# Optimization experiments

Measured on AMD Instinct MI355X. Metric: run time of the kernel, lower is better.

The kernel has to match this reference:

```python
import jax, jax.numpy as jnp
import numpy as np

B, T, DIM = 8, 1024, 512
H, DK, L = 8, 64, 32          # heads, dim_key, rel_pos_length
DH = H * DK                    # dim_hidden = 512
DOUT = 512
EPS = 1e-5


def setup_inputs() -> dict:
    key = jax.random.key(0)
    ks = jax.random.split(key, 5)
    x = jax.random.normal(ks[0], (B, T, DIM), jnp.float32)
    Wqkv = jax.random.normal(ks[1], (3 * DH, DIM), jnp.float32) * (1.0 / np.sqrt(DIM))
    Wout = jax.random.normal(ks[2], (DOUT, DH), jnp.float32) * (1.0 / np.sqrt(DH))
    bout = jax.random.normal(ks[3], (DOUT,), jnp.float32) * 0.01
    rel_positions = jax.random.normal(ks[4], (2 * L - 1, DK), jnp.float32)
    bn_gamma = jnp.ones((DK,), jnp.float32)
    bn_beta = jnp.zeros((DK,), jnp.float32)
    return {"x": x, "Wqkv": Wqkv, "Wout": Wout, "bout": bout,
            "rel_positions": rel_positions, "bn_gamma": bn_gamma, "bn_beta": bn_beta}


def reference(x, Wqkv, Wout, bout, rel_positions, bn_gamma, bn_beta):
    b, t, f = x.shape
    # Conv1d(dim, 3*dim_hidden, 1, bias=False) on x.transpose(1,2) == pointwise matmul
    qkv = jnp.einsum('btf,of->bot', x, Wqkv)          # (b, 3*DH, t)
    q, k, v = jnp.split(qkv, 3, axis=1)
    q = q.reshape(b * H, DK, t)
    k = k.reshape(b * H, DK, t)
    v = v.reshape(b * H, DK, t)

    # linear-attention core: softmax over sequence for k, tiny DKxDK context
    k = jax.nn.softmax(k, axis=-1)
    context = jnp.einsum('ndt,net->nde', k, v)        # (n, DK, DK)
    content_out = jnp.einsum('nde,ndt->net', context, q)  # (n, DK, t); norm_queries=False

    # Relative-position path. Original builds one-hot It (t,t,2L-1) and
    # Pt = einsum('tir,rd->tid', It, rel_positions); then
    # St = einsum('ndt,tid->nit', q, Pt); rel = einsum('nit,net->net', St, v)
    #     = v * (sum_i St)[:,None,:].
    # sum_i Pt[t,i,d] = sum over valid band offsets of rel_positions -> band matmul.
    r = jnp.arange(-(L - 1), L)                       # (2L-1,)
    pos = jnp.arange(t)
    tgt = pos[:, None] + r[None, :]                   # i = x + r
    valid = ((tgt >= 0) & (tgt < t)).astype(x.dtype)  # (t, 2L-1)
    Psum = valid @ rel_positions                      # (t, DK) == Pt.sum(axis=1)
    S = jnp.einsum('ndt,td->nt', q, Psum)             # (n, t)
    rel = v * S[:, None, :]                           # (n, DK, t)

    # BatchNorm1d(DK), training-mode batch stats over (n, t), biased variance
    mu = jnp.mean(rel, axis=(0, 2), keepdims=True)
    var = jnp.mean((rel - mu) ** 2, axis=(0, 2), keepdims=True)
    rel = (rel - mu) * jax.lax.rsqrt(var + EPS) * bn_gamma[None, :, None] + bn_beta[None, :, None]

    out = (content_out + rel).reshape(b, DH, t)
    # Conv1d(dim_hidden, dim_out, 1) with bias
    return jnp.einsum('od,bdt->bot', Wout, out) + bout[None, :, None]
```

## Files before the change

kernel.cpp:

```cpp
#include <hip/hip_runtime.h>
#include <hip/hip_bf16.h>


typedef short bf16x8 __attribute__((ext_vector_type(8)));
typedef float f32x4 __attribute__((ext_vector_type(4)));

static __device__ __forceinline__ unsigned short f2bf(float f) {
  __hip_bfloat16 h = __float2bfloat16(f);
  return *reinterpret_cast<unsigned short*>(&h);
}
static __device__ __forceinline__ float bf2f(unsigned short u) {
  union { unsigned int i; float f; } c; c.i = ((unsigned int)u) << 16;
  return c.f;
}
static __device__ __forceinline__ void gl_lds16(const unsigned short* g, unsigned short* l) {
  __builtin_amdgcn_global_load_lds((const __attribute__((address_space(1))) unsigned int*)g,
                                   (__attribute__((address_space(3))) unsigned int*)l,
                                   16, 0, 0);
}

__global__ __launch_bounds__(256) void cast_all(const float* __restrict__ x,
                                                const float* __restrict__ wqkv,
                                                const float* __restrict__ wout,
                                                unsigned short* __restrict__ xb,
                                                unsigned short* __restrict__ wqkvb,
                                                unsigned short* __restrict__ woutb) {
  int j = blockIdx.x * 256 + threadIdx.x;
  const float* src; unsigned short* dst;
  if (j < 1048576) { src = x; dst = xb; }
  else if (j < 1245184) { j -= 1048576; src = wqkv; dst = wqkvb; }
  else { j -= 1245184; src = wout; dst = woutb; }
  float4 v = ((const float4*)src)[j];
  ushort4 o = {f2bf(v.x), f2bf(v.y), f2bf(v.z), f2bf(v.w)};
  ((ushort4*)dst)[j] = o;
}


__global__ __launch_bounds__(256) void gemm_qkv(const unsigned short* __restrict__ A,
                                                const unsigned short* __restrict__ B,
                                                unsigned short* __restrict__ C) {
  __shared__ alignas(16) unsigned short As[4096];
  __shared__ alignas(16) unsigned short Bs[4096];
  const int tid = threadIdx.x;
  const int wave = tid >> 6, lane = tid & 63;
  const int bm = blockIdx.y * 128, bn = blockIdx.x * 128;
  const int wm = (wave >> 1) * 64, wn = (wave & 1) * 64;
  const int fr = lane & 15, cq = lane >> 4;
  const int ch0 = tid, ch1 = 256 + tid;
  const int r0 = ch0 >> 2, c0 = (ch0 & 3) ^ ((r0 >> 1) & 3);
  const int r1 = ch1 >> 2, c1 = (ch1 & 3) ^ ((r1 >> 1) & 3);
  unsigned short* la0 = As + (wave * 64) * 8;
  unsigned short* la1 = As + (256 + wave * 64) * 8;
  unsigned short* lb0 = Bs + (wave * 64) * 8;
  unsigned short* lb1 = Bs + (256 + wave * 64) * 8;
  const unsigned short* Ar0 = A + (size_t)(bm + r0) * 512 + c0 * 8;
  const unsigned short* Ar1 = A + (size_t)(bm + r1) * 512 + c1 * 8;
  const unsigned short* Br0 = B + (size_t)(bn + r0) * 512 + c0 * 8;
  const unsigned short* Br1 = B + (size_t)(bn + r1) * 512 + c1 * 8;
  int offA[4], offB[4];
#pragma unroll
  for (int i = 0; i < 4; ++i) {
    int ra = wm + i * 16 + fr;
    offA[i] = (ra * 4 + (cq ^ ((ra >> 1) & 3))) * 8;
    int rb = wn + i * 16 + fr;
    offB[i] = (rb * 4 + (cq ^ ((rb >> 1) & 3))) * 8;
  }
  f32x4 acc[4][4];
#pragma unroll
  for (int i = 0; i < 4; ++i)
#pragma unroll
    for (int j = 0; j < 4; ++j) acc[i][j] = (f32x4){0.f, 0.f, 0.f, 0.f};
  for (int k0 = 0; k0 < 512; k0 += 32) {
    __syncthreads();
    gl_lds16(Ar0 + k0, la0);
    gl_lds16(Ar1 + k0, la1);
    gl_lds16(Br0 + k0, lb0);
    gl_lds16(Br1 + k0, lb1);
    __builtin_amdgcn_s_waitcnt(0);
    __syncthreads();
    bf16x8 af[4], bq[4];
#pragma unroll
    for (int mi = 0; mi < 4; ++mi) af[mi] = *(const bf16x8*)(As + offA[mi]);
#pragma unroll
    for (int nj = 0; nj < 4; ++nj) bq[nj] = *(const bf16x8*)(Bs + offB[nj]);
#pragma unroll
    for (int mi = 0; mi < 4; ++mi)
#pragma unroll
      for (int nj = 0; nj < 4; ++nj)
        acc[mi][nj] = __builtin_amdgcn_mfma_f32_16x16x32_bf16(af[mi], bq[nj], acc[mi][nj], 0, 0, 0);
  }
#pragma unroll
  for (int mi = 0; mi < 4; ++mi) {
    const int row0 = bm + wm + mi * 16 + (lane >> 4) * 4;
#pragma unroll
    for (int nj = 0; nj < 4; ++nj) {
      const int col = bn + wn + nj * 16 + fr;
#pragma unroll
      for (int rr = 0; rr < 4; ++rr)
        C[(size_t)(row0 + rr) * 8192 + col] = f2bf(acc[mi][nj][rr]);
    }
  }
}

__global__ __launch_bounds__(256) void gemm_out(const unsigned short* __restrict__ A,
                                                const unsigned short* __restrict__ B,
                                                const float* __restrict__ bias,
                                                float* __restrict__ out) {
  __shared__ alignas(16) unsigned short As[4096];
  __shared__ alignas(16) unsigned short Bs[4096];
  const int tid = threadIdx.x;
  const int wave = tid >> 6, lane = tid & 63;
  const int bm = blockIdx.y * 128, bn = blockIdx.x * 128;
  const int wm = (wave >> 1) * 64, wn = (wave & 1) * 64;
  const int fr = lane & 15, cq = lane >> 4;
  const int ch0 = tid, ch1 = 256 + tid;
  const int r0 = ch0 >> 2, c0 = (ch0 & 3) ^ ((r0 >> 1) & 3);
  const int r1 = ch1 >> 2, c1 = (ch1 & 3) ^ ((r1 >> 1) & 3);
  unsigned short* la0 = As + (wave * 64) * 8;
  unsigned short* la1 = As + (256 + wave * 64) * 8;
  unsigned short* lb0 = Bs + (wave * 64) * 8;
  unsigned short* lb1 = Bs + (256 + wave * 64) * 8;
  const unsigned short* Ar0 = A + (size_t)(bm + r0) * 512 + c0 * 8;
  const unsigned short* Ar1 = A + (size_t)(bm + r1) * 512 + c1 * 8;
  const unsigned short* Br0 = B + (size_t)(bn + r0) * 512 + c0 * 8;
  const unsigned short* Br1 = B + (size_t)(bn + r1) * 512 + c1 * 8;
  int offA[4], offB[4];
#pragma unroll
  for (int i = 0; i < 4; ++i) {
    int ra = wm + i * 16 + fr;
    offA[i] = (ra * 4 + (cq ^ ((ra >> 1) & 3))) * 8;
    int rb = wn + i * 16 + fr;
    offB[i] = (rb * 4 + (cq ^ ((rb >> 1) & 3))) * 8;
  }
  f32x4 acc[4][4];
#pragma unroll
  for (int i = 0; i < 4; ++i)
#pragma unroll
    for (int j = 0; j < 4; ++j) acc[i][j] = (f32x4){0.f, 0.f, 0.f, 0.f};
  for (int k0 = 0; k0 < 512; k0 += 32) {
    __syncthreads();
    gl_lds16(Ar0 + k0, la0);
    gl_lds16(Ar1 + k0, la1);
    gl_lds16(Br0 + k0, lb0);
    gl_lds16(Br1 + k0, lb1);
    __builtin_amdgcn_s_waitcnt(0);
    __syncthreads();
    bf16x8 af[4], bq[4];
#pragma unroll
    for (int mi = 0; mi < 4; ++mi) af[mi] = *(const bf16x8*)(As + offA[mi]);
#pragma unroll
    for (int nj = 0; nj < 4; ++nj) bq[nj] = *(const bf16x8*)(Bs + offB[nj]);
#pragma unroll
    for (int mi = 0; mi < 4; ++mi)
#pragma unroll
      for (int nj = 0; nj < 4; ++nj)
        acc[mi][nj] = __builtin_amdgcn_mfma_f32_16x16x32_bf16(af[mi], bq[nj], acc[mi][nj], 0, 0, 0);
  }
#pragma unroll
  for (int mi = 0; mi < 4; ++mi) {
    const int row0 = bm + wm + mi * 16 + (lane >> 4) * 4;
#pragma unroll
    for (int nj = 0; nj < 4; ++nj) {
      const int col = bn + wn + nj * 16 + fr;
      const int b = col >> 10, t = col & 1023;
#pragma unroll
      for (int rr = 0; rr < 4; ++rr)
        out[(size_t)b * 524288 + (size_t)(row0 + rr) * 1024 + t] = acc[mi][nj][rr] + bias[row0 + rr];
    }
  }
}

__global__ __launch_bounds__(256) void kstats(const unsigned short* __restrict__ qkv,
                                              float* __restrict__ lse) {
  const int tid = threadIdx.x;
  const int wave = tid >> 6, lane = tid & 63;
  const int r = blockIdx.x * 4 + wave;
  const int hd = r >> 3, b = r & 7;
  const unsigned short* row = qkv + (size_t)(512 + hd) * 8192 + b * 1024 + lane * 16;
  uint4 u0 = *(const uint4*)row;
  uint4 u1 = *(const uint4*)(row + 8);
  const unsigned short* us0 = (const unsigned short*)&u0;
  const unsigned short* us1 = (const unsigned short*)&u1;
  float f[16];
#pragma unroll
  for (int i = 0; i < 8; ++i) { f[i] = bf2f(us0[i]); f[8 + i] = bf2f(us1[i]); }
  float m = f[0];
#pragma unroll
  for (int i = 1; i < 16; ++i) m = fmaxf(m, f[i]);
#pragma unroll
  for (int off = 32; off; off >>= 1) m = fmaxf(m, __shfl_xor(m, off));
  float s = 0.f;
#pragma unroll
  for (int i = 0; i < 16; ++i) s += __expf(f[i] - m);
#pragma unroll
  for (int off = 32; off; off >>= 1) s += __shfl_xor(s, off);
  if (lane == 0) lse[r] = m + __logf(s);
}

__global__ __launch_bounds__(256) void psum_kernel(const float* __restrict__ relpos,
                                                   float* __restrict__ PsumT) {
  const int d = blockIdx.y;
  const int t = blockIdx.x * 256 + threadIdx.x;
  float acc = 0.f;
  for (int j = 0; j < 63; ++j) {
    int i = t + j - 31;
    float v = relpos[j * 64 + d];
    if (i >= 0 && i < 1024) acc += v;
  }
  PsumT[d * 1024 + t] = acc;
}

__global__ __launch_bounds__(256) void context_mfma(const unsigned short* __restrict__ qkv,
                                                    const float* __restrict__ lse,
                                                    float* __restrict__ ctx_part) {
  const int tc = blockIdx.x, n = blockIdx.y;
  const int b = n >> 3, h = n & 7;
  const int tid = threadIdx.x;
  const int wave = tid >> 6, lane = tid & 63;
  __shared__ float ls[64];
  __shared__ float ctx_l[64][68];
  if (tid < 64) ls[tid] = lse[(h * 64 + tid) * 8 + b];
  __syncthreads();
  const int fr = lane & 15, fk = (lane >> 4) * 8;
  const size_t colbase = (size_t)b * 1024 + tc * 256 + wave * 64;
  const unsigned short* kbase = qkv + (size_t)(512 + h * 64) * 8192 + colbase;
  const unsigned short* vbase = qkv + (size_t)(1024 + h * 64) * 8192 + colbase;
  f32x4 acc[4][4];
#pragma unroll
  for (int i = 0; i < 4; ++i)
#pragma unroll
    for (int j = 0; j < 4; ++j) acc[i][j] = (f32x4){0.f, 0.f, 0.f, 0.f};
#pragma unroll
  for (int ks = 0; ks < 2; ++ks) {
    const int tb = ks * 32 + fk;
    bf16x8 aF[4], bF[4];
#pragma unroll
    for (int dt = 0; dt < 4; ++dt) {
      const int row = dt * 16 + fr;
      bf16x8 kv = *(const bf16x8*)(kbase + (size_t)row * 8192 + tb);
      const float lv = ls[row];
      bf16x8 pv;
#pragma unroll
      for (int j = 0; j < 8; ++j)
        pv[j] = (short)f2bf(__expf(bf2f((unsigned short)kv[j]) - lv));
      aF[dt] = pv;
    }
#pragma unroll
    for (int et = 0; et < 4; ++et)
      bF[et] = *(const bf16x8*)(vbase + (size_t)(et * 16 + fr) * 8192 + tb);
#pragma unroll
    for (int dt = 0; dt < 4; ++dt)
#pragma unroll
      for (int et = 0; et < 4; ++et)
        acc[dt][et] = __builtin_amdgcn_mfma_f32_16x16x32_bf16(aF[dt], bF[et], acc[dt][et], 0, 0, 0);
  }
#pragma unroll
  for (int w = 0; w < 4; ++w) {
    if (wave == w) {
#pragma unroll
      for (int dt = 0; dt < 4; ++dt)
#pragma unroll
        for (int et = 0; et < 4; ++et) {
          const int col = et * 16 + fr;
#pragma unroll
          for (int rr = 0; rr < 4; ++rr) {
            const int rw = dt * 16 + (lane >> 4) * 4 + rr;
            if (w == 0) ctx_l[rw][col] = acc[dt][et][rr];
            else ctx_l[rw][col] += acc[dt][et][rr];
          }
        }
    }
    __syncthreads();
  }
  float* outp = ctx_part + ((size_t)tc * 64 + n) * 4096;
  for (int i = tid * 4; i < 4096; i += 1024) {
    const int rw = i >> 6, cc = i & 63;
    *(float4*)(outp + i) = *(const float4*)&ctx_l[rw][cc];
  }
}

__global__ __launch_bounds__(256) void reduce_ctx(const float* __restrict__ part,
                                                  float* __restrict__ ctx) {
  const int i4 = blockIdx.x * 256 + threadIdx.x;
  const float4* p = (const float4*)part;
  float4 a = p[i4], b = p[65536 + i4], c = p[131072 + i4], d = p[196608 + i4];
  float4 s = {a.x + b.x + c.x + d.x, a.y + b.y + c.y + d.y,
              a.z + b.z + c.z + d.z, a.w + b.w + c.w + d.w};
  ((float4*)ctx)[i4] = s;
}

__global__ __launch_bounds__(256) void s_stats(const unsigned short* __restrict__ qkv,
                                               const float* __restrict__ PsumT,
                                               float* __restrict__ S,
                                               float* __restrict__ part1,
                                               float* __restrict__ part2) {
  const int tc = blockIdx.x, n = blockIdx.y;
  const int b = n >> 3, h = n & 7;
  const int t0 = tc * 64;
  const int tid = threadIdx.x, wave = tid >> 6, lane = tid & 63;
  const int tg = lane & 7, rg = lane >> 3;
  __shared__ float swave[4][64];
  __shared__ float s_lds[64];
  const unsigned short* qbase = qkv + (size_t)(h * 64) * 8192 + b * 1024 + t0 + tg * 8;
  const float* pbase = PsumT + t0 + tg * 8;
  float acc[8] = {0.f};
#pragma unroll
  for (int i = 0; i < 2; ++i) {
    const int d = wave * 16 + i * 8 + rg;
    bf16x8 qv = *(const bf16x8*)(qbase + (size_t)d * 8192);
    float4 p0 = *(const float4*)(pbase + d * 1024);
    float4 p1 = *(const float4*)(pbase + d * 1024 + 4);
    float p[8] = {p0.x, p0.y, p0.z, p0.w, p1.x, p1.y, p1.z, p1.w};
#pragma unroll
    for (int j = 0; j < 8; ++j) acc[j] = fmaf(bf2f((unsigned short)qv[j]), p[j], acc[j]);
  }
#pragma unroll
  for (int off = 8; off < 64; off <<= 1)
#pragma unroll
    for (int j = 0; j < 8; ++j) acc[j] += __shfl_xor(acc[j], off);
  if (rg == 0) {
#pragma unroll
    for (int j = 0; j < 8; ++j) swave[wave][tg * 8 + j] = acc[j];
  }
  __syncthreads();
  if (tid < 64) {
    float s = swave[0][tid] + swave[1][tid] + swave[2][tid] + swave[3][tid];
    s_lds[tid] = s;
    S[(size_t)n * 1024 + t0 + tid] = s;
  }
  __syncthreads();
  const unsigned short* vbase = qkv + (size_t)(1024 + h * 64) * 8192 + b * 1024 + t0 + tg * 8;
  const int blk = n * 16 + tc;
  float sv[8];
#pragma unroll
  for (int j = 0; j < 8; ++j) sv[j] = s_lds[tg * 8 + j];
#pragma unroll
  for (int i = 0; i < 2; ++i) {
    const int e = wave * 16 + i * 8 + rg;
    bf16x8 vv = *(const bf16x8*)(vbase + (size_t)e * 8192);
    float a1 = 0.f, a2 = 0.f;
#pragma unroll
    for (int j = 0; j < 8; ++j) {
      float val = bf2f((unsigned short)vv[j]) * sv[j];
      a1 += val;
      a2 = fmaf(val, val, a2);
    }
#pragma unroll
    for (int off = 1; off < 8; off <<= 1) {
      a1 += __shfl_xor(a1, off);
      a2 += __shfl_xor(a2, off);
    }
    if (tg == 0) {
      part1[e * 1024 + blk] = a1;
      part2[e * 1024 + blk] = a2;
    }
  }
}

__global__ __launch_bounds__(256) void bn_reduce(const float* __restrict__ part1,
                                                 const float* __restrict__ part2,
                                                 const float* __restrict__ gamma,
                                                 const float* __restrict__ beta,
                                                 float* __restrict__ scale,
                                                 float* __restrict__ shift) {
  const int e = blockIdx.x;
  const int tid = threadIdx.x;
  float a1 = 0.f, a2 = 0.f;
#pragma unroll
  for (int i = 0; i < 4; ++i) {
    a1 += part1[e * 1024 + i * 256 + tid];
    a2 += part2[e * 1024 + i * 256 + tid];
  }
#pragma unroll
  for (int off = 32; off; off >>= 1) {
    a1 += __shfl_down(a1, off);
    a2 += __shfl_down(a2, off);
  }
  __shared__ float r1[4], r2[4];
  const int w = tid >> 6, lane = tid & 63;
  if (lane == 0) { r1[w] = a1; r2[w] = a2; }
  __syncthreads();
  if (tid == 0) {
    float s1 = r1[0] + r1[1] + r1[2] + r1[3];
    float s2 = r2[0] + r2[1] + r2[2] + r2[3];
    const float cnt = 65536.0f;
    float mu = s1 / cnt;
    float var = s2 / cnt - mu * mu;
    float sc = gamma[e] * rsqrtf(var + 1e-5f);
    scale[e] = sc;
    shift[e] = beta[e] - mu * sc;
  }
}

__global__ __launch_bounds__(256) void content_out_t(const unsigned short* __restrict__ qkv,
                                                     const float* __restrict__ ctx,
                                                     const float* __restrict__ S,
                                                     const float* __restrict__ scale,
                                                     const float* __restrict__ shift,
                                                     unsigned short* __restrict__ outT) {
  const int chunk = blockIdx.x, n = blockIdx.y;
  const int b = n >> 3, h = n & 7;
  const int t0 = chunk * 64;
  __shared__ float cs[4096];
  __shared__ alignas(16) unsigned short T[64][72];
  const float* cp = ctx + (size_t)n * 4096;
  for (int i = threadIdx.x * 4; i < 4096; i += 1024)
    *(float4*)&cs[i] = *(const float4*)&cp[i];
  __syncthreads();
  const int tid = threadIdx.x;
  const int e0 = (tid & 15) * 4;
  const int tq = (tid >> 4) * 4;
  const unsigned short* qbase = qkv + (size_t)(h * 64) * 8192 + b * 1024 + t0 + tq;
  float acc[4][4] = {{0.f}};
  for (int d = 0; d < 64; ++d) {
    float4 cv = *(const float4*)&cs[d * 64 + e0];
    ushort4 qu = *(const ushort4*)(qbase + (size_t)d * 8192);
    float qa[4] = {bf2f(qu.x), bf2f(qu.y), bf2f(qu.z), bf2f(qu.w)};
    float ca[4] = {cv.x, cv.y, cv.z, cv.w};
#pragma unroll
    for (int a = 0; a < 4; ++a)
#pragma unroll
      for (int c = 0; c < 4; ++c)
        acc[a][c] = fmaf(ca[a], qa[c], acc[a][c]);
  }
  float4 svv = *(const float4*)(S + (size_t)n * 1024 + t0 + tq);
  float sa[4] = {svv.x, svv.y, svv.z, svv.w};
  float4 scv = *(const float4*)(scale + e0);
  float4 shv = *(const float4*)(shift + e0);
  float sc[4] = {scv.x, scv.y, scv.z, scv.w};
  float sh[4] = {shv.x, shv.y, shv.z, shv.w};
#pragma unroll
  for (int a = 0; a < 4; ++a) {
    ushort4 vu = *(const ushort4*)(qkv + (size_t)(1024 + h * 64 + e0 + a) * 8192 + b * 1024 + t0 + tq);
    float va[4] = {bf2f(vu.x), bf2f(vu.y), bf2f(vu.z), bf2f(vu.w)};
#pragma unroll
    for (int c = 0; c < 4; ++c)
      T[tq + c][e0 + a] = f2bf(fmaf(va[c] * sa[c], sc[a], acc[a][c] + sh[a]));
  }
  __syncthreads();
  const int tl = tid >> 2, dq = (tid & 3) * 16;
  uint4 r0 = *(uint4*)&T[tl][dq];
  uint4 r1 = *(uint4*)&T[tl][dq + 8];
  unsigned short* op = outT + ((size_t)(b * 1024 + t0 + tl)) * 512 + h * 64 + dq;
  *(uint4*)op = r0;
  *(uint4*)(op + 8) = r1;
}

extern "C" void kernel_launch(void* const* d_in, const int* in_sizes, int n_in,
                              void* d_out, int out_size, void* d_ws, size_t ws_size,
                              hipStream_t stream) {
  const float* x       = (const float*)d_in[0];
  const float* Wqkv    = (const float*)d_in[1];
  const float* Wout    = (const float*)d_in[2];
  const float* bout    = (const float*)d_in[3];
  const float* relpos  = (const float*)d_in[4];
  const float* gamma   = (const float*)d_in[5];
  const float* beta    = (const float*)d_in[6];
  float* out = (float*)d_out;

  float* ws = (float*)d_ws;
  unsigned short* qkvb  = (unsigned short*)ws;
  float* p = ws + 6291456;
  unsigned short* xb    = (unsigned short*)p;  p += 2097152;
  unsigned short* wqkvb = (unsigned short*)p;  p += 393216;
  unsigned short* woutb = (unsigned short*)p;  p += 131072;
  float* ctx_part = p;  p += 1048576;
  float* ctx      = p;  p += 262144;
  float* PsumT    = p;  p += 65536;
  float* S        = p;  p += 65536;
  float* lse      = p;  p += 4096;
  float* part1    = p;  p += 65536;
  float* part2    = p;  p += 65536;
  float* scale    = p;  p += 64;
  float* shift    = p;  p += 64;
  unsigned short* outT = (unsigned short*)p;

  cast_all<<<5120, 256, 0, stream>>>(x, Wqkv, Wout, xb, wqkvb, woutb);
  psum_kernel<<<dim3(4, 64), 256, 0, stream>>>(relpos, PsumT);
  gemm_qkv<<<dim3(64, 12), 256, 0, stream>>>(wqkvb, xb, qkvb);
  kstats<<<1024, 256, 0, stream>>>(qkvb, lse);
  s_stats<<<dim3(16, 64), 256, 0, stream>>>(qkvb, PsumT, S, part1, part2);
  bn_reduce<<<64, 256, 0, stream>>>(part1, part2, gamma, beta, scale, shift);
  context_mfma<<<dim3(4, 64), 256, 0, stream>>>(qkvb, lse, ctx_part);
  reduce_ctx<<<256, 256, 0, stream>>>(ctx_part, ctx);
  content_out_t<<<dim3(16, 64), 256, 0, stream>>>(qkvb, ctx, S, scale, shift, outT);
  gemm_out<<<dim3(64, 4), 256, 0, stream>>>(woutb, outT, bout, out);
}
```

Baseline: 165.3 us.

## Merge independent launches into combined kernels and double GEMM K-tile to 64

```diff
diff --git a/kernel.cpp b/kernel.cpp
--- a/kernel.cpp
+++ b/kernel.cpp
@@ -19,75 +19,96 @@
                                    16, 0, 0);
 }
 
-__global__ __launch_bounds__(256) void cast_all(const float* __restrict__ x,
-                                                const float* __restrict__ wqkv,
-                                                const float* __restrict__ wout,
-                                                unsigned short* __restrict__ xb,
-                                                unsigned short* __restrict__ wqkvb,
-                                                unsigned short* __restrict__ woutb) {
-  int j = blockIdx.x * 256 + threadIdx.x;
-  const float* src; unsigned short* dst;
-  if (j < 1048576) { src = x; dst = xb; }
-  else if (j < 1245184) { j -= 1048576; src = wqkv; dst = wqkvb; }
-  else { j -= 1245184; src = wout; dst = woutb; }
-  float4 v = ((const float4*)src)[j];
-  ushort4 o = {f2bf(v.x), f2bf(v.y), f2bf(v.z), f2bf(v.w)};
-  ((ushort4*)dst)[j] = o;
+__global__ __launch_bounds__(256) void prep(const float* __restrict__ x,
+                                            const float* __restrict__ wqkv,
+                                            const float* __restrict__ wout,
+                                            const float* __restrict__ relpos,
+                                            unsigned short* __restrict__ xb,
+                                            unsigned short* __restrict__ wqkvb,
+                                            unsigned short* __restrict__ woutb,
+                                            float* __restrict__ PsumT) {
+  const int bx = blockIdx.x;
+  if (bx < 5120) {
+    int j = bx * 256 + threadIdx.x;
+    const float* src; unsigned short* dst;
+    if (j < 1048576) { src = x; dst = xb; }
+    else if (j < 1245184) { j -= 1048576; src = wqkv; dst = wqkvb; }
+    else { j -= 1245184; src = wout; dst = woutb; }
+    float4 v = ((const float4*)src)[j];
+    ushort4 o = {f2bf(v.x), f2bf(v.y), f2bf(v.z), f2bf(v.w)};
+    ((ushort4*)dst)[j] = o;
+  } else {
+    const int idx = bx - 5120;
+    const int d = idx >> 2;
+    const int t = (idx & 3) * 256 + threadIdx.x;
+    float acc = 0.f;
+    for (int j = 0; j < 63; ++j) {
+      int i = t + j - 31;
+      float v = relpos[j * 64 + d];
+      if (i >= 0 && i < 1024) acc += v;
+    }
+    PsumT[d * 1024 + t] = acc;
+  }
 }
 
 
 __global__ __launch_bounds__(256) void gemm_qkv(const unsigned short* __restrict__ A,
                                                 const unsigned short* __restrict__ B,
                                                 unsigned short* __restrict__ C) {
-  __shared__ alignas(16) unsigned short As[4096];
-  __shared__ alignas(16) unsigned short Bs[4096];
+  __shared__ alignas(16) unsigned short As[8192];
+  __shared__ alignas(16) unsigned short Bs[8192];
   const int tid = threadIdx.x;
   const int wave = tid >> 6, lane = tid & 63;
   const int bm = blockIdx.y * 128, bn = blockIdx.x * 128;
   const int wm = (wave >> 1) * 64, wn = (wave & 1) * 64;
   const int fr = lane & 15, cq = lane >> 4;
-  const int ch0 = tid, ch1 = 256 + tid;
-  const int r0 = ch0 >> 2, c0 = (ch0 & 3) ^ ((r0 >> 1) & 3);
-  const int r1 = ch1 >> 2, c1 = (ch1 & 3) ^ ((r1 >> 1) & 3);
-  unsigned short* la0 = As + (wave * 64) * 8;
-  unsigned short* la1 = As + (256 + wave * 64) * 8;
-  unsigned short* lb0 = Bs + (wave * 64) * 8;
-  unsigned short* lb1 = Bs + (256 + wave * 64) * 8;
-  const unsigned short* Ar0 = A + (size_t)(bm + r0) * 512 + c0 * 8;
-  const unsigned short* Ar1 = A + (size_t)(bm + r1) * 512 + c1 * 8;
-  const unsigned short* Br0 = B + (size_t)(bn + r0) * 512 + c0 * 8;
-  const unsigned short* Br1 = B + (size_t)(bn + r1) * 512 + c1 * 8;
-  int offA[4], offB[4];
-#pragma unroll
-  for (int i = 0; i < 4; ++i) {
-    int ra = wm + i * 16 + fr;
-    offA[i] = (ra * 4 + (cq ^ ((ra >> 1) & 3))) * 8;
-    int rb = wn + i * 16 + fr;
-    offB[i] = (rb * 4 + (cq ^ ((rb >> 1) & 3))) * 8;
-  }
+  const unsigned short* srcA[4];
+  const unsigned short* srcB[4];
+#pragma unroll
+  for (int j = 0; j < 4; ++j) {
+    const int s = tid + j * 256;
+    const int row = s >> 3, cp = s & 7;
+    const int c = cp ^ (row & 7);
+    srcA[j] = A + (size_t)(bm + row) * 512 + c * 8;
+    srcB[j] = B + (size_t)(bn + row) * 512 + c * 8;
+  }
+  int offA[4][2], offB[4][2];
+#pragma unroll
+  for (int i = 0; i < 4; ++i)
+#pragma unroll
+    for (int ks = 0; ks < 2; ++ks) {
+      int ra = wm + i * 16 + fr;
+      offA[i][ks] = (ra * 8 + ((ks * 4 + cq) ^ (ra & 7))) * 8;
+      int rb = wn + i * 16 + fr;
+      offB[i][ks] = (rb * 8 + ((ks * 4 + cq) ^ (rb & 7))) * 8;
+    }
   f32x4 acc[4][4];
 #pragma unroll
   for (int i = 0; i < 4; ++i)
 #pragma unroll
     for (int j = 0; j < 4; ++j) acc[i][j] = (f32x4){0.f, 0.f, 0.f, 0.f};
-  for (int k0 = 0; k0 < 512; k0 += 32) {
-    __syncthreads();
-    gl_lds16(Ar0 + k0, la0);
-    gl_lds16(Ar1 + k0, la1);
-    gl_lds16(Br0 + k0, lb0);
-    gl_lds16(Br1 + k0, lb1);
+  for (int k0 = 0; k0 < 512; k0 += 64) {
+    __syncthreads();
+#pragma unroll
+    for (int j = 0; j < 4; ++j) {
+      gl_lds16(srcA[j] + k0, As + (wave * 64 + j * 256) * 8);
+      gl_lds16(srcB[j] + k0, Bs + (wave * 64 + j * 256) * 8);
+    }
     __builtin_amdgcn_s_waitcnt(0);
     __syncthreads();
-    bf16x8 af[4], bq[4];
-#pragma unroll
-    for (int mi = 0; mi < 4; ++mi) af[mi] = *(const bf16x8*)(As + offA[mi]);
-#pragma unroll
-    for (int nj = 0; nj < 4; ++nj) bq[nj] = *(const bf16x8*)(Bs + offB[nj]);
-#pragma unroll
-    for (int mi = 0; mi < 4; ++mi)
-#pragma unroll
-      for (int nj = 0; nj < 4; ++nj)
-        acc[mi][nj] = __builtin_amdgcn_mfma_f32_16x16x32_bf16(af[mi], bq[nj], acc[mi][nj], 0, 0, 0);
+#pragma unroll
+    for (int ks = 0; ks < 2; ++ks) {
+      bf16x8 af[4], bq[4];
+#pragma unroll
+      for (int mi = 0; mi < 4; ++mi) af[mi] = *(const bf16x8*)(As + offA[mi][ks]);
+#pragma unroll
+      for (int nj = 0; nj < 4; ++nj) bq[nj] = *(const bf16x8*)(Bs + offB[nj][ks]);
+#pragma unroll
+      for (int mi = 0; mi < 4; ++mi)
+#pragma unroll
+        for (int nj = 0; nj < 4; ++nj)
+          acc[mi][nj] = __builtin_amdgcn_mfma_f32_16x16x32_bf16(af[mi], bq[nj], acc[mi][nj], 0, 0, 0);
+    }
   }
 #pragma unroll
   for (int mi = 0; mi < 4; ++mi) {
@@ -106,55 +127,60 @@
                                                 const unsigned short* __restrict__ B,
                                                 const float* __restrict__ bias,
                                                 float* __restrict__ out) {
-  __shared__ alignas(16) unsigned short As[4096];
-  __shared__ alignas(16) unsigned short Bs[4096];
+  __shared__ alignas(16) unsigned short As[8192];
+  __shared__ alignas(16) unsigned short Bs[8192];
   const int tid = threadIdx.x;
   const int wave = tid >> 6, lane = tid & 63;
   const int bm = blockIdx.y * 128, bn = blockIdx.x * 128;
   const int wm = (wave >> 1) * 64, wn = (wave & 1) * 64;
   const int fr = lane & 15, cq = lane >> 4;
-  const int ch0 = tid, ch1 = 256 + tid;
-  const int r0 = ch0 >> 2, c0 = (ch0 & 3) ^ ((r0 >> 1) & 3);
-  const int r1 = ch1 >> 2, c1 = (ch1 & 3) ^ ((r1 >> 1) & 3);
-  unsigned short* la0 = As + (wave * 64) * 8;
-  unsigned short* la1 = As + (256 + wave * 64) * 8;
-  unsigned short* lb0 = Bs + (wave * 64) * 8;
-  unsigned short* lb1 = Bs + (256 + wave * 64) * 8;
-  const unsigned short* Ar0 = A + (size_t)(bm + r0) * 512 + c0 * 8;
-  const unsigned short* Ar1 = A + (size_t)(bm + r1) * 512 + c1 * 8;
-  const unsigned short* Br0 = B + (size_t)(bn + r0) * 512 + c0 * 8;
-  const unsigned short* Br1 = B + (size_t)(bn + r1) * 512 + c1 * 8;
-  int offA[4], offB[4];
-#pragma unroll
-  for (int i = 0; i < 4; ++i) {
-    int ra = wm + i * 16 + fr;
-    offA[i] = (ra * 4 + (cq ^ ((ra >> 1) & 3))) * 8;
-    int rb = wn + i * 16 + fr;
-    offB[i] = (rb * 4 + (cq ^ ((rb >> 1) & 3))) * 8;
-  }
+  const unsigned short* srcA[4];
+  const unsigned short* srcB[4];
+#pragma unroll
+  for (int j = 0; j < 4; ++j) {
+    const int s = tid + j * 256;
+    const int row = s >> 3, cp = s & 7;
+    const int c = cp ^ (row & 7);
+    srcA[j] = A + (size_t)(bm + row) * 512 + c * 8;
+    srcB[j] = B + (size_t)(bn + row) * 512 + c * 8;
+  }
+  int offA[4][2], offB[4][2];
+#pragma unroll
+  for (int i = 0; i < 4; ++i)
+#pragma unroll
+    for (int ks = 0; ks < 2; ++ks) {
+      int ra = wm + i * 16 + fr;
+      offA[i][ks] = (ra * 8 + ((ks * 4 + cq) ^ (ra & 7))) * 8;
+      int rb = wn + i * 16 + fr;
+      offB[i][ks] = (rb * 8 + ((ks * 4 + cq) ^ (rb & 7))) * 8;
+    }
   f32x4 acc[4][4];
 #pragma unroll
   for (int i = 0; i < 4; ++i)
 #pragma unroll
     for (int j = 0; j < 4; ++j) acc[i][j] = (f32x4){0.f, 0.f, 0.f, 0.f};
-  for (int k0 = 0; k0 < 512; k0 += 32) {
-    __syncthreads();
-    gl_lds16(Ar0 + k0, la0);
-    gl_lds16(Ar1 + k0, la1);
-    gl_lds16(Br0 + k0, lb0);
-    gl_lds16(Br1 + k0, lb1);
+  for (int k0 = 0; k0 < 512; k0 += 64) {
+    __syncthreads();
+#pragma unroll
+    for (int j = 0; j < 4; ++j) {
+      gl_lds16(srcA[j] + k0, As + (wave * 64 + j * 256) * 8);
+      gl_lds16(srcB[j] + k0, Bs + (wave * 64 + j * 256) * 8);
+    }
     __builtin_amdgcn_s_waitcnt(0);
     __syncthreads();
-    bf16x8 af[4], bq[4];
-#pragma unroll
-    for (int mi = 0; mi < 4; ++mi) af[mi] = *(const bf16x8*)(As + offA[mi]);
-#pragma unroll
-    for (int nj = 0; nj < 4; ++nj) bq[nj] = *(const bf16x8*)(Bs + offB[nj]);
-#pragma unroll
-    for (int mi = 0; mi < 4; ++mi)
-#pragma unroll
-      for (int nj = 0; nj < 4; ++nj)
-        acc[mi][nj] = __builtin_amdgcn_mfma_f32_16x16x32_bf16(af[mi], bq[nj], acc[mi][nj], 0, 0, 0);
+#pragma unroll
+    for (int ks = 0; ks < 2; ++ks) {
+      bf16x8 af[4], bq[4];
+#pragma unroll
+      for (int mi = 0; mi < 4; ++mi) af[mi] = *(const bf16x8*)(As + offA[mi][ks]);
+#pragma unroll
+      for (int nj = 0; nj < 4; ++nj) bq[nj] = *(const bf16x8*)(Bs + offB[nj][ks]);
+#pragma unroll
+      for (int mi = 0; mi < 4; ++mi)
+#pragma unroll
+        for (int nj = 0; nj < 4; ++nj)
+          acc[mi][nj] = __builtin_amdgcn_mfma_f32_16x16x32_bf16(af[mi], bq[nj], acc[mi][nj], 0, 0, 0);
+    }
   }
 #pragma unroll
   for (int mi = 0; mi < 4; ++mi) {
@@ -170,44 +196,98 @@
   }
 }
 
-__global__ __launch_bounds__(256) void kstats(const unsigned short* __restrict__ qkv,
-                                              float* __restrict__ lse) {
-  const int tid = threadIdx.x;
-  const int wave = tid >> 6, lane = tid & 63;
-  const int r = blockIdx.x * 4 + wave;
-  const int hd = r >> 3, b = r & 7;
-  const unsigned short* row = qkv + (size_t)(512 + hd) * 8192 + b * 1024 + lane * 16;
-  uint4 u0 = *(const uint4*)row;
-  uint4 u1 = *(const uint4*)(row + 8);
-  const unsigned short* us0 = (const unsigned short*)&u0;
-  const unsigned short* us1 = (const unsigned short*)&u1;
-  float f[16];
-#pragma unroll
-  for (int i = 0; i < 8; ++i) { f[i] = bf2f(us0[i]); f[8 + i] = bf2f(us1[i]); }
-  float m = f[0];
-#pragma unroll
-  for (int i = 1; i < 16; ++i) m = fmaxf(m, f[i]);
-#pragma unroll
-  for (int off = 32; off; off >>= 1) m = fmaxf(m, __shfl_xor(m, off));
-  float s = 0.f;
-#pragma unroll
-  for (int i = 0; i < 16; ++i) s += __expf(f[i] - m);
-#pragma unroll
-  for (int off = 32; off; off >>= 1) s += __shfl_xor(s, off);
-  if (lane == 0) lse[r] = m + __logf(s);
-}
-
-__global__ __launch_bounds__(256) void psum_kernel(const float* __restrict__ relpos,
-                                                   float* __restrict__ PsumT) {
-  const int d = blockIdx.y;
-  const int t = blockIdx.x * 256 + threadIdx.x;
-  float acc = 0.f;
-  for (int j = 0; j < 63; ++j) {
-    int i = t + j - 31;
-    float v = relpos[j * 64 + d];
-    if (i >= 0 && i < 1024) acc += v;
-  }
-  PsumT[d * 1024 + t] = acc;
+__global__ __launch_bounds__(256) void stats(const unsigned short* __restrict__ qkv,
+                                             const float* __restrict__ PsumT,
+                                             float* __restrict__ S,
+                                             float* __restrict__ part1,
+                                             float* __restrict__ part2,
+                                             float* __restrict__ lse) {
+  const int bx = blockIdx.x;
+  const int tid = threadIdx.x, wave = tid >> 6, lane = tid & 63;
+  __shared__ float swave[4][64];
+  __shared__ float s_lds[64];
+  if (bx < 1024) {
+    const int tc = bx & 15, n = bx >> 4;
+    const int b = n >> 3, h = n & 7;
+    const int t0 = tc * 64;
+    const int tg = lane & 7, rg = lane >> 3;
+    const unsigned short* qbase = qkv + (size_t)(h * 64) * 8192 + b * 1024 + t0 + tg * 8;
+    const float* pbase = PsumT + t0 + tg * 8;
+    float acc[8] = {0.f};
+#pragma unroll
+    for (int i = 0; i < 2; ++i) {
+      const int d = wave * 16 + i * 8 + rg;
+      bf16x8 qv = *(const bf16x8*)(qbase + (size_t)d * 8192);
+      float4 p0 = *(const float4*)(pbase + d * 1024);
+      float4 p1 = *(const float4*)(pbase + d * 1024 + 4);
+      float p[8] = {p0.x, p0.y, p0.z, p0.w, p1.x, p1.y, p1.z, p1.w};
+#pragma unroll
+      for (int j = 0; j < 8; ++j) acc[j] = fmaf(bf2f((unsigned short)qv[j]), p[j], acc[j]);
+    }
+#pragma unroll
+    for (int off = 8; off < 64; off <<= 1)
+#pragma unroll
+      for (int j = 0; j < 8; ++j) acc[j] += __shfl_xor(acc[j], off);
+    if (rg == 0) {
+#pragma unroll
+      for (int j = 0; j < 8; ++j) swave[wave][tg * 8 + j] = acc[j];
+    }
+    __syncthreads();
+    if (tid < 64) {
+      float s = swave[0][tid] + swave[1][tid] + swave[2][tid] + swave[3][tid];
+      s_lds[tid] = s;
+      S[(size_t)n * 1024 + t0 + tid] = s;
+    }
+    __syncthreads();
+    const unsigned short* vbase = qkv + (size_t)(1024 + h * 64) * 8192 + b * 1024 + t0 + tg * 8;
+    const int blk = n * 16 + tc;
+    float sv[8];
+#pragma unroll
+    for (int j = 0; j < 8; ++j) sv[j] = s_lds[tg * 8 + j];
+#pragma unroll
+    for (int i = 0; i < 2; ++i) {
+      const int e = wave * 16 + i * 8 + rg;
+      bf16x8 vv = *(const bf16x8*)(vbase + (size_t)e * 8192);
+      float a1 = 0.f, a2 = 0.f;
+#pragma unroll
+      for (int j = 0; j < 8; ++j) {
+        float val = bf2f((unsigned short)vv[j]) * sv[j];
+        a1 += val;
+        a2 = fmaf(val, val, a2);
+      }
+#pragma unroll
+      for (int off = 1; off < 8; off <<= 1) {
+        a1 += __shfl_xor(a1, off);
+        a2 += __shfl_xor(a2, off);
+      }
+      if (tg == 0) {
+        part1[e * 1024 + blk] = a1;
+        part2[e * 1024 + blk] = a2;
+      }
+    }
+  } else {
+    const int r = (bx - 1024) * 4 + wave;
+    const int hd = r >> 3, b = r & 7;
+    const unsigned short* row = qkv + (size_t)(512 + hd) * 8192 + b * 1024 + lane * 16;
+    uint4 u0 = *(const uint4*)row;
+    uint4 u1 = *(const uint4*)(row + 8);
+    const unsigned short* us0 = (const unsigned short*)&u0;
+    const unsigned short* us1 = (const unsigned short*)&u1;
+    float f[16];
+#pragma unroll
+    for (int i = 0; i < 8; ++i) { f[i] = bf2f(us0[i]); f[8 + i] = bf2f(us1[i]); }
+    float m = f[0];
+#pragma unroll
+    for (int i = 1; i < 16; ++i) m = fmaxf(m, f[i]);
+#pragma unroll
+    for (int off = 32; off; off >>= 1) m = fmaxf(m, __shfl_xor(m, off));
+    float s = 0.f;
+#pragma unroll
+    for (int i = 0; i < 16; ++i) s += __expf(f[i] - m);
+#pragma unroll
+    for (int off = 32; off; off >>= 1) s += __shfl_xor(s, off);
+    if (lane == 0) lse[r] = m + __logf(s);
+  }
 }
 
 __global__ __launch_bounds__(256) void context_mfma(const unsigned short* __restrict__ qkv,
@@ -279,116 +359,50 @@
   }
 }
 
-__global__ __launch_bounds__(256) void reduce_ctx(const float* __restrict__ part,
-                                                  float* __restrict__ ctx) {
-  const int i4 = blockIdx.x * 256 + threadIdx.x;
-  const float4* p = (const float4*)part;
-  float4 a = p[i4], b = p[65536 + i4], c = p[131072 + i4], d = p[196608 + i4];
-  float4 s = {a.x + b.x + c.x + d.x, a.y + b.y + c.y + d.y,
-              a.z + b.z + c.z + d.z, a.w + b.w + c.w + d.w};
-  ((float4*)ctx)[i4] = s;
-}
-
-__global__ __launch_bounds__(256) void s_stats(const unsigned short* __restrict__ qkv,
-                                               const float* __restrict__ PsumT,
-                                               float* __restrict__ S,
-                                               float* __restrict__ part1,
-                                               float* __restrict__ part2) {
-  const int tc = blockIdx.x, n = blockIdx.y;
-  const int b = n >> 3, h = n & 7;
-  const int t0 = tc * 64;
-  const int tid = threadIdx.x, wave = tid >> 6, lane = tid & 63;
-  const int tg = lane & 7, rg = lane >> 3;
-  __shared__ float swave[4][64];
-  __shared__ float s_lds[64];
-  const unsigned short* qbase = qkv + (size_t)(h * 64) * 8192 + b * 1024 + t0 + tg * 8;
-  const float* pbase = PsumT + t0 + tg * 8;
-  float acc[8] = {0.f};
-#pragma unroll
-  for (int i = 0; i < 2; ++i) {
-    const int d = wave * 16 + i * 8 + rg;
-    bf16x8 qv = *(const bf16x8*)(qbase + (size_t)d * 8192);
-    float4 p0 = *(const float4*)(pbase + d * 1024);
-    float4 p1 = *(const float4*)(pbase + d * 1024 + 4);
-    float p[8] = {p0.x, p0.y, p0.z, p0.w, p1.x, p1.y, p1.z, p1.w};
-#pragma unroll
-    for (int j = 0; j < 8; ++j) acc[j] = fmaf(bf2f((unsigned short)qv[j]), p[j], acc[j]);
-  }
-#pragma unroll
-  for (int off = 8; off < 64; off <<= 1)
-#pragma unroll
-    for (int j = 0; j < 8; ++j) acc[j] += __shfl_xor(acc[j], off);
-  if (rg == 0) {
-#pragma unroll
-    for (int j = 0; j < 8; ++j) swave[wave][tg * 8 + j] = acc[j];
-  }
-  __syncthreads();
-  if (tid < 64) {
-    float s = swave[0][tid] + swave[1][tid] + swave[2][tid] + swave[3][tid];
-    s_lds[tid] = s;
-    S[(size_t)n * 1024 + t0 + tid] = s;
-  }
-  __syncthreads();
-  const unsigned short* vbase = qkv + (size_t)(1024 + h * 64) * 8192 + b * 1024 + t0 + tg * 8;
-  const int blk = n * 16 + tc;
-  float sv[8];
-#pragma unroll
-  for (int j = 0; j < 8; ++j) sv[j] = s_lds[tg * 8 + j];
-#pragma unroll
-  for (int i = 0; i < 2; ++i) {
-    const int e = wave * 16 + i * 8 + rg;
-    bf16x8 vv = *(const bf16x8*)(vbase + (size_t)e * 8192);
+__global__ __launch_bounds__(256) void reduce2(const float* __restrict__ part,
+                                               float* __restrict__ ctx,
+                                               const float* __restrict__ part1,
+                                               const float* __restrict__ part2,
+                                               const float* __restrict__ gamma,
+                                               const float* __restrict__ beta,
+                                               float* __restrict__ scale,
+                                               float* __restrict__ shift) {
+  const int bx = blockIdx.x;
+  const int tid = threadIdx.x;
+  if (bx < 256) {
+    const int i4 = bx * 256 + tid;
+    const float4* p = (const float4*)part;
+    float4 a = p[i4], b = p[65536 + i4], c = p[131072 + i4], d = p[196608 + i4];
+    float4 s = {a.x + b.x + c.x + d.x, a.y + b.y + c.y + d.y,
+                a.z + b.z + c.z + d.z, a.w + b.w + c.w + d.w};
+    ((float4*)ctx)[i4] = s;
+  } else {
+    const int e = bx - 256;
     float a1 = 0.f, a2 = 0.f;
 #pragma unroll
-    for (int j = 0; j < 8; ++j) {
-      float val = bf2f((unsigned short)vv[j]) * sv[j];
-      a1 += val;
-      a2 = fmaf(val, val, a2);
-    }
-#pragma unroll
-    for (int off = 1; off < 8; off <<= 1) {
-      a1 += __shfl_xor(a1, off);
-      a2 += __shfl_xor(a2, off);
-    }
-    if (tg == 0) {
-      part1[e * 1024 + blk] = a1;
-      part2[e * 1024 + blk] = a2;
-    }
-  }
-}
-
-__global__ __launch_bounds__(256) void bn_reduce(const float* __restrict__ part1,
-                                                 const float* __restrict__ part2,
-                                                 const float* __restrict__ gamma,
-                                                 const float* __restrict__ beta,
-                                                 float* __restrict__ scale,
-                                                 float* __restrict__ shift) {
-  const int e = blockIdx.x;
-  const int tid = threadIdx.x;
-  float a1 = 0.f, a2 = 0.f;
-#pragma unroll
-  for (int i = 0; i < 4; ++i) {
-    a1 += part1[e * 1024 + i * 256 + tid];
-    a2 += part2[e * 1024 + i * 256 + tid];
-  }
-#pragma unroll
-  for (int off = 32; off; off >>= 1) {
-    a1 += __shfl_down(a1, off);
-    a2 += __shfl_down(a2, off);
-  }
-  __shared__ float r1[4], r2[4];
-  const int w = tid >> 6, lane = tid & 63;
-  if (lane == 0) { r1[w] = a1; r2[w] = a2; }
-  __syncthreads();
-  if (tid == 0) {
-    float s1 = r1[0] + r1[1] + r1[2] + r1[3];
-    float s2 = r2[0] + r2[1] + r2[2] + r2[3];
-    const float cnt = 65536.0f;
-    float mu = s1 / cnt;
-    float var = s2 / cnt - mu * mu;
-    float sc = gamma[e] * rsqrtf(var + 1e-5f);
-    scale[e] = sc;
-    shift[e] = beta[e] - mu * sc;
+    for (int i = 0; i < 4; ++i) {
+      a1 += part1[e * 1024 + i * 256 + tid];
+      a2 += part2[e * 1024 + i * 256 + tid];
+    }
+#pragma unroll
+    for (int off = 32; off; off >>= 1) {
+      a1 += __shfl_down(a1, off);
+      a2 += __shfl_down(a2, off);
+    }
+    __shared__ float r1[4], r2[4];
+    const int w = tid >> 6, lane = tid & 63;
+    if (lane == 0) { r1[w] = a1; r2[w] = a2; }
+    __syncthreads();
+    if (tid == 0) {
+      float s1 = r1[0] + r1[1] + r1[2] + r1[3];
+      float s2 = r2[0] + r2[1] + r2[2] + r2[3];
+      const float cnt = 65536.0f;
+      float mu = s1 / cnt;
+      float var = s2 / cnt - mu * mu;
+      float sc = gamma[e] * rsqrtf(var + 1e-5f);
+      scale[e] = sc;
+      shift[e] = beta[e] - mu * sc;
+    }
   }
 }
 
@@ -475,14 +489,11 @@
   float* shift    = p;  p += 64;
   unsigned short* outT = (unsigned short*)p;
 
-  cast_all<<<5120, 256, 0, stream>>>(x, Wqkv, Wout, xb, wqkvb, woutb);
-  psum_kernel<<<dim3(4, 64), 256, 0, stream>>>(relpos, PsumT);
+  prep<<<5376, 256, 0, stream>>>(x, Wqkv, Wout, relpos, xb, wqkvb, woutb, PsumT);
   gemm_qkv<<<dim3(64, 12), 256, 0, stream>>>(wqkvb, xb, qkvb);
-  kstats<<<1024, 256, 0, stream>>>(qkvb, lse);
-  s_stats<<<dim3(16, 64), 256, 0, stream>>>(qkvb, PsumT, S, part1, part2);
-  bn_reduce<<<64, 256, 0, stream>>>(part1, part2, gamma, beta, scale, shift);
+  stats<<<2048, 256, 0, stream>>>(qkvb, PsumT, S, part1, part2, lse);
   context_mfma<<<dim3(4, 64), 256, 0, stream>>>(qkvb, lse, ctx_part);
-  reduce_ctx<<<256, 256, 0, stream>>>(ctx_part, ctx);
+  reduce2<<<320, 256, 0, stream>>>(ctx_part, ctx, part1, part2, gamma, beta, scale, shift);
   content_out_t<<<dim3(16, 64), 256, 0, stream>>>(qkvb, ctx, S, scale, shift, outT);
   gemm_out<<<dim3(64, 4), 256, 0, stream>>>(woutb, outT, bout, out);
 }
```

Measured after the change: 163.3 us. No clear change (-1.2%).
